# Kernel tuning notes

Hardware: AMD Instinct MI355X
Metric: run time of the kernel (lower is better)

## Reference

```python
import jax, jax.numpy as jnp
import numpy as np

DT = 1.0
SEQ, BATCH, HID = 2048, 512, 256

def setup_inputs() -> dict:
    key = jax.random.key(0)
    ks = jax.random.split(key, 4)
    x = jax.random.normal(ks[0], (SEQ, BATCH, 1), dtype=jnp.float32)
    # small init scale keeps tanh unsaturated and the Euler recurrence stable
    W1 = 0.3 * jax.random.normal(ks[1], (2, HID), dtype=jnp.float32)
    b1 = jnp.zeros((HID,), jnp.float32)
    W2 = (0.3 / np.sqrt(HID)) * jax.random.normal(ks[2], (HID, HID), dtype=jnp.float32)
    b2 = jnp.zeros((HID,), jnp.float32)
    W3 = (0.1 / np.sqrt(HID)) * jax.random.normal(ks[3], (HID, 1), dtype=jnp.float32)
    b3 = jnp.zeros((1,), jnp.float32)
    state0 = jnp.zeros((BATCH,), jnp.float32)
    return {"x": x, "W1": W1, "b1": b1, "W2": W2, "b2": b2, "W3": W3, "b3": b3, "state0": state0}

def reference(x, W1, b1, W2, b2, W3, b3, state0):
    # Forward-Euler ODE integration: y[n+1] = y[n] + dt * f(x[n], y[n]).
    # Torch code returns odeint_output[:-1, :, None], i.e. the state at each
    # step BEFORE the update, with shape identical to x.
    xs = x[:, :, 0]  # (seq, batch) -- derivative_network.input = x.squeeze(2)

    def f(x_t, y):
        u = jnp.stack([x_t, y], axis=-1)          # (B, 2)
        h = jnp.tanh(u @ W1 + b1)                 # (B, H)
        h = jnp.tanh(h @ W2 + b2)                 # (B, H)
        return (h @ W3 + b3)[:, 0]                # (B,)

    def step(state, x_t):
        new_state = state + DT * f(x_t, state)
        return new_state, state                   # emit pre-update state

    _, ys = jax.lax.scan(step, state0, xs)        # ys: (seq, batch)
    return ys[:, :, None]                         # (seq, batch, 1), same shape as x
```

## Files before the change

### kernel.cpp

```cpp
#include <hip/hip_runtime.h>


#define SEQ 2048
#define BATCH 512
#define HID 256

typedef __bf16 bf16x8 __attribute__((ext_vector_type(8)));
typedef short short8 __attribute__((ext_vector_type(8)));
typedef float f32x4 __attribute__((ext_vector_type(4)));

__device__ __forceinline__ unsigned short f2bf_rne(float f) {
  unsigned u = __builtin_bit_cast(unsigned, f);
  u += 0x7fffu + ((u >> 16) & 1u);
  return (unsigned short)(u >> 16);
}

__device__ __forceinline__ float tanh_pade(float x) {
  float cx = __builtin_amdgcn_fmed3f(x, -4.5f, 4.5f);
  float u = cx * cx;
  float num = cx * (10395.f + u * (1260.f + 21.f * u));
  float den = 10395.f + u * (4725.f + u * (210.f + u));
  return num * __builtin_amdgcn_rcpf(den);
}

__device__ __forceinline__ float row16_sum_to_lane15(float v) {
  int s;
  s = __builtin_amdgcn_update_dpp(0, __builtin_bit_cast(int, v), 0x111, 0xf, 0xf, true);
  v += __builtin_bit_cast(float, s);
  s = __builtin_amdgcn_update_dpp(0, __builtin_bit_cast(int, v), 0x112, 0xf, 0xf, true);
  v += __builtin_bit_cast(float, s);
  s = __builtin_amdgcn_update_dpp(0, __builtin_bit_cast(int, v), 0x114, 0xf, 0xf, true);
  v += __builtin_bit_cast(float, s);
  s = __builtin_amdgcn_update_dpp(0, __builtin_bit_cast(int, v), 0x118, 0xf, 0xf, true);
  v += __builtin_bit_cast(float, s);
  return v;
}

__global__ void pack_w2_kernel(const float* __restrict__ W2,
                               unsigned short* __restrict__ ws) {
  int idx = blockIdx.x * 256 + threadIdx.x;
  int e    = idx & 7;
  int l    = (idx >> 3) & 63;
  int kc   = (idx >> 9) & 7;
  int tile = idx >> 12;
  int k = kc * 32 + (l >> 4) * 8 + e;
  int c = tile * 16 + (l & 15);
  ws[idx] = f2bf_rne(W2[k * HID + c]);
}

__global__ __launch_bounds__(256, 1) void odenet_kernel(
    const float* __restrict__ x, const float* __restrict__ W1,
    const float* __restrict__ b1, const unsigned short* __restrict__ wsW2,
    const float* __restrict__ b2, const float* __restrict__ W3,
    const float* __restrict__ b3, const float* __restrict__ state0,
    float* __restrict__ out) {
  __shared__ __align__(16) unsigned short A_lds[2 * HID];
  __shared__ __align__(16) float partial[2][4];

  const int tid  = threadIdx.x;
  const int lane = tid & 63;
  const int wave = tid >> 6;
  const int j    = tid;
  const int b0   = blockIdx.x * 2;

  const float w10 = W1[j];
  const float w11 = W1[HID + j];
  const float b1j = b1[j];
  const float b3v = b3[0];
  float b2c[4], w3c[4];
#pragma unroll
  for (int t = 0; t < 4; ++t) {
    const int c = wave * 64 + t * 16 + (lane & 15);
    b2c[t] = b2[c];
    w3c[t] = W3[c];
  }

  short8 bf[4][8];
  {
    const short8* wp = (const short8*)wsW2;
#pragma unroll
    for (int t = 0; t < 4; ++t)
#pragma unroll
      for (int kc = 0; kc < 8; ++kc)
        bf[t][kc] = wp[((wave * 4 + t) * 8 + kc) * 64 + lane];
  }

  const short8 zero8 = {0, 0, 0, 0, 0, 0, 0, 0};
  short8 areg[8];
#pragma unroll
  for (int kc = 0; kc < 8; ++kc) areg[kc] = zero8;
  const bool aread = ((lane & 11) == 0);
  const int  arow  = (lane >> 2) & 1;
  const int  aoff  = arow * HID + (lane >> 4) * 8;

  float y0 = state0[b0];
  float y1 = state0[b0 + 1];

  const float* xp = x + b0;
  float* yo = out + b0;

  float2 xb[8], xn[8];
  float xa0[8], xa1[8];
#pragma unroll
  for (int i = 0; i < 8; ++i) xb[i] = *(const float2*)&xp[i * BATCH];
#pragma unroll
  for (int i = 0; i < 8; ++i) {
    xa0[i] = xb[i].x * w10 + b1j;
    xa1[i] = xb[i].y * w10 + b1j;
  }

  for (int tb = 0; tb < SEQ; tb += 8) {
    if (tb + 8 < SEQ) {
      const float* xq = xp + (tb + 8) * BATCH;
#pragma unroll
      for (int i = 0; i < 8; ++i) xn[i] = *(const float2*)&xq[i * BATCH];
    }

#pragma unroll
    for (int i = 0; i < 8; ++i) {
      const int t = tb + i;

      const float pre0 = __builtin_fmaf(y0, w11, xa0[i]);
      const float pre1 = __builtin_fmaf(y1, w11, xa1[i]);
      A_lds[j]       = f2bf_rne(tanh_pade(pre0));
      A_lds[HID + j] = f2bf_rne(tanh_pade(pre1));
      __syncthreads();

      if (aread) {
#pragma unroll
        for (int kc = 0; kc < 8; ++kc)
          areg[kc] = *(const short8*)&A_lds[aoff + kc * 32];
      }

      f32x4 acc[4];
#pragma unroll
      for (int t4 = 0; t4 < 4; ++t4) acc[t4] = f32x4{0.f, 0.f, 0.f, 0.f};
#pragma unroll
      for (int kc = 0; kc < 8; ++kc) {
        const bf16x8 a = __builtin_bit_cast(bf16x8, areg[kc]);
#pragma unroll
        for (int t4 = 0; t4 < 4; ++t4)
          acc[t4] = __builtin_amdgcn_mfma_f32_16x16x32_bf16(
              a, __builtin_bit_cast(bf16x8, bf[t4][kc]), acc[t4], 0, 0, 0);
      }

      float s = 0.f;
      if (lane < 32) {
#pragma unroll
        for (int t4 = 0; t4 < 4; ++t4)
          s += tanh_pade(acc[t4][0] + b2c[t4]) * w3c[t4];
      }
      s = row16_sum_to_lane15(s);
      if ((lane & 15) == 15 && lane < 32)
        partial[lane >> 4][wave] = s;
      __syncthreads();

      const f32x4 q0 = *(const f32x4*)&partial[0][0];
      const f32x4 q1 = *(const f32x4*)&partial[1][0];
      const float f0 = ((q0[0] + q0[1]) + (q0[2] + q0[3])) + b3v;
      const float f1 = ((q1[0] + q1[1]) + (q1[2] + q1[3])) + b3v;
      const float y0o = y0, y1o = y1;
      y0 += f0;
      y1 += f1;
      if (tid == 0) {
        float2 o{y0o, y1o};
        *(float2*)&yo[t * BATCH] = o;
      }
    }

    if (tb + 8 < SEQ) {
#pragma unroll
      for (int i = 0; i < 8; ++i) xb[i] = xn[i];
#pragma unroll
      for (int i = 0; i < 8; ++i) {
        xa0[i] = xb[i].x * w10 + b1j;
        xa1[i] = xb[i].y * w10 + b1j;
      }
    }
  }
}

extern "C" void kernel_launch(void* const* d_in, const int* in_sizes, int n_in,
                              void* d_out, int out_size, void* d_ws, size_t ws_size,
                              hipStream_t stream) {
  const float* x  = (const float*)d_in[0];
  const float* W1 = (const float*)d_in[1];
  const float* b1 = (const float*)d_in[2];
  const float* W2 = (const float*)d_in[3];
  const float* b2 = (const float*)d_in[4];
  const float* W3 = (const float*)d_in[5];
  const float* b3 = (const float*)d_in[6];
  const float* s0 = (const float*)d_in[7];
  unsigned short* ws = (unsigned short*)d_ws;
  float* out = (float*)d_out;

  pack_w2_kernel<<<256, 256, 0, stream>>>(W2, ws);
  odenet_kernel<<<256, 256, 0, stream>>>(x, W1, b1, ws, b2, W3, b3, s0, out);
}
```

Measured before the change: 1.445 ms.

## Assign one batch element per block and launch twice as many blocks

Each block now integrates a single batch element instead of two, so the grid grows to 512 blocks. Launch bounds are raised to two blocks per CU so that two independent recurrences can share a CU and hide each other's barrier and MFMA latency. Per step this halves the tanh and LDS-write work, and the x prefetch unroll drops from 8 to 4. The cost is that the W2 fragments are now loaded and held in registers by twice as many blocks, and the register cap that comes with two blocks per CU could cause spills.

```diff
diff --git a/kernel.cpp b/kernel.cpp
--- a/kernel.cpp
+++ b/kernel.cpp
@@ -48,20 +48,20 @@
   ws[idx] = f2bf_rne(W2[k * HID + c]);
 }
 
-__global__ __launch_bounds__(256, 1) void odenet_kernel(
+__global__ __launch_bounds__(256, 2) void odenet_kernel(
     const float* __restrict__ x, const float* __restrict__ W1,
     const float* __restrict__ b1, const unsigned short* __restrict__ wsW2,
     const float* __restrict__ b2, const float* __restrict__ W3,
     const float* __restrict__ b3, const float* __restrict__ state0,
     float* __restrict__ out) {
-  __shared__ __align__(16) unsigned short A_lds[2 * HID];
-  __shared__ __align__(16) float partial[2][4];
+  __shared__ __align__(16) unsigned short A_lds[HID];
+  __shared__ __align__(16) float partial[4];
 
   const int tid  = threadIdx.x;
   const int lane = tid & 63;
   const int wave = tid >> 6;
   const int j    = tid;
-  const int b0   = blockIdx.x * 2;
+  const int b0   = blockIdx.x;
 
   const float w10 = W1[j];
   const float w11 = W1[HID + j];
@@ -89,41 +89,33 @@
   short8 areg[8];
 #pragma unroll
   for (int kc = 0; kc < 8; ++kc) areg[kc] = zero8;
-  const bool aread = ((lane & 11) == 0);
-  const int  arow  = (lane >> 2) & 1;
-  const int  aoff  = arow * HID + (lane >> 4) * 8;
+  const bool aread = ((lane & 15) == 0);
+  const int  aoff  = (lane >> 4) * 8;
 
-  float y0 = state0[b0];
-  float y1 = state0[b0 + 1];
+  const f32x4 kZero = {0.f, 0.f, 0.f, 0.f};
+
+  float y = state0[b0];
 
   const float* xp = x + b0;
   float* yo = out + b0;
 
-  float2 xb[8], xn[8];
-  float xa0[8], xa1[8];
+  float xb[4], xn[4];
 #pragma unroll
-  for (int i = 0; i < 8; ++i) xb[i] = *(const float2*)&xp[i * BATCH];
+  for (int i = 0; i < 4; ++i) xb[i] = xp[i * BATCH];
+
+  for (int tb = 0; tb < SEQ; tb += 4) {
+    if (tb + 4 < SEQ) {
+      const float* xq = xp + (tb + 4) * BATCH;
 #pragma unroll
-  for (int i = 0; i < 8; ++i) {
-    xa0[i] = xb[i].x * w10 + b1j;
-    xa1[i] = xb[i].y * w10 + b1j;
-  }
-
-  for (int tb = 0; tb < SEQ; tb += 8) {
-    if (tb + 8 < SEQ) {
-      const float* xq = xp + (tb + 8) * BATCH;
-#pragma unroll
-      for (int i = 0; i < 8; ++i) xn[i] = *(const float2*)&xq[i * BATCH];
+      for (int i = 0; i < 4; ++i) xn[i] = xq[i * BATCH];
     }
 
 #pragma unroll
-    for (int i = 0; i < 8; ++i) {
+    for (int i = 0; i < 4; ++i) {
       const int t = tb + i;
 
-      const float pre0 = __builtin_fmaf(y0, w11, xa0[i]);
-      const float pre1 = __builtin_fmaf(y1, w11, xa1[i]);
-      A_lds[j]       = f2bf_rne(tanh_pade(pre0));
-      A_lds[HID + j] = f2bf_rne(tanh_pade(pre1));
+      const float pre = __builtin_fmaf(y, w11, __builtin_fmaf(xb[i], w10, b1j));
+      A_lds[j] = f2bf_rne(tanh_pade(pre));
       __syncthreads();
 
       if (aread) {
@@ -132,50 +124,44 @@
           areg[kc] = *(const short8*)&A_lds[aoff + kc * 32];
       }
 
-      f32x4 acc[4];
+      f32x4 acc0, acc1, acc2, acc3;
+      {
+        const bf16x8 a = __builtin_bit_cast(bf16x8, areg[0]);
+        acc0 = __builtin_amdgcn_mfma_f32_16x16x32_bf16(a, __builtin_bit_cast(bf16x8, bf[0][0]), kZero, 0, 0, 0);
+        acc1 = __builtin_amdgcn_mfma_f32_16x16x32_bf16(a, __builtin_bit_cast(bf16x8, bf[1][0]), kZero, 0, 0, 0);
+        acc2 = __builtin_amdgcn_mfma_f32_16x16x32_bf16(a, __builtin_bit_cast(bf16x8, bf[2][0]), kZero, 0, 0, 0);
+        acc3 = __builtin_amdgcn_mfma_f32_16x16x32_bf16(a, __builtin_bit_cast(bf16x8, bf[3][0]), kZero, 0, 0, 0);
+      }
 #pragma unroll
-      for (int t4 = 0; t4 < 4; ++t4) acc[t4] = f32x4{0.f, 0.f, 0.f, 0.f};
-#pragma unroll
-      for (int kc = 0; kc < 8; ++kc) {
+      for (int kc = 1; kc < 8; ++kc) {
         const bf16x8 a = __builtin_bit_cast(bf16x8, areg[kc]);
-#pragma unroll
-        for (int t4 = 0; t4 < 4; ++t4)
-          acc[t4] = __builtin_amdgcn_mfma_f32_16x16x32_bf16(
-              a, __builtin_bit_cast(bf16x8, bf[t4][kc]), acc[t4], 0, 0, 0);
+        acc0 = __builtin_amdgcn_mfma_f32_16x16x32_bf16(a, __builtin_bit_cast(bf16x8, bf[0][kc]), acc0, 0, 0, 0);
+        acc1 = __builtin_amdgcn_mfma_f32_16x16x32_bf16(a, __builtin_bit_cast(bf16x8, bf[1][kc]), acc1, 0, 0, 0);
+        acc2 = __builtin_amdgcn_mfma_f32_16x16x32_bf16(a, __builtin_bit_cast(bf16x8, bf[2][kc]), acc2, 0, 0, 0);
+        acc3 = __builtin_amdgcn_mfma_f32_16x16x32_bf16(a, __builtin_bit_cast(bf16x8, bf[3][kc]), acc3, 0, 0, 0);
       }
 
       float s = 0.f;
-      if (lane < 32) {
-#pragma unroll
-        for (int t4 = 0; t4 < 4; ++t4)
-          s += tanh_pade(acc[t4][0] + b2c[t4]) * w3c[t4];
+      if (lane < 16) {
+        s  = tanh_pade(acc0[0] + b2c[0]) * w3c[0];
+        s += tanh_pade(acc1[0] + b2c[1]) * w3c[1];
+        s += tanh_pade(acc2[0] + b2c[2]) * w3c[2];
+        s += tanh_pade(acc3[0] + b2c[3]) * w3c[3];
       }
       s = row16_sum_to_lane15(s);
-      if ((lane & 15) == 15 && lane < 32)
-        partial[lane >> 4][wave] = s;
+      if (lane == 15) partial[wave] = s;
       __syncthreads();
 
-      const f32x4 q0 = *(const f32x4*)&partial[0][0];
-      const f32x4 q1 = *(const f32x4*)&partial[1][0];
-      const float f0 = ((q0[0] + q0[1]) + (q0[2] + q0[3])) + b3v;
-      const float f1 = ((q1[0] + q1[1]) + (q1[2] + q1[3])) + b3v;
-      const float y0o = y0, y1o = y1;
-      y0 += f0;
-      y1 += f1;
-      if (tid == 0) {
-        float2 o{y0o, y1o};
-        *(float2*)&yo[t * BATCH] = o;
-      }
+      const f32x4 q = *(const f32x4*)&partial[0];
+      const float f = ((q[0] + q[1]) + (q[2] + q[3])) + b3v;
+      const float y_old = y;
+      y += f;
+      if (tid == 0) yo[t * BATCH] = y_old;
     }
 
-    if (tb + 8 < SEQ) {
+    if (tb + 4 < SEQ) {
 #pragma unroll
-      for (int i = 0; i < 8; ++i) xb[i] = xn[i];
-#pragma unroll
-      for (int i = 0; i < 8; ++i) {
-        xa0[i] = xb[i].x * w10 + b1j;
-        xa1[i] = xb[i].y * w10 + b1j;
-      }
+      for (int i = 0; i < 4; ++i) xb[i] = xn[i];
     }
   }
 }
@@ -195,5 +181,5 @@
   float* out = (float*)d_out;
 
   pack_w2_kernel<<<256, 256, 0, stream>>>(W2, ws);
-  odenet_kernel<<<256, 256, 0, stream>>>(x, W1, b1, ws, b2, W3, b3, s0, out);
+  odenet_kernel<<<512, 256, 0, stream>>>(x, W1, b1, ws, b2, W3, b3, s0, out);
 }
```

Measured after the change: 1.562 ms. 1.08x slower.
